# Kernel optimization log

Hardware: AMD Instinct MI355X
Metric: run time of the kernel (lower is better)

Reference implementation:

```python
import jax, jax.numpy as jnp
import numpy as np

B, C, H, W = 8, 64, 128, 128


def setup_inputs() -> dict:
    key = jax.random.key(0)
    k1, k2, k3 = jax.random.split(key, 3)
    x = jax.random.normal(k1, (B, C, H, W), dtype=jnp.float32)
    # offset conv weights: (2C, C, 3, 3), small init like the module (std=0.01)
    W_off = jax.random.normal(k2, (2 * C, C, 3, 3), dtype=jnp.float32) * 0.01
    # following regular conv: (C_out, C, 3, 3)
    W_conv = jax.random.normal(k3, (C, C, 3, 3), dtype=jnp.float32) * 0.05
    b_conv = jnp.zeros((C,), dtype=jnp.float32)
    return {"x": x, "W_off": W_off, "W_conv": W_conv, "b_conv": b_conv}


def _conv2d_same(x, w):
    return jax.lax.conv_general_dilated(
        x, w, window_strides=(1, 1), padding=[(1, 1), (1, 1)],
        dimension_numbers=("NCHW", "OIHW", "NCHW"))


def _deform_offset(x, W_off):
    """Faithful ConvOffset2D: offset conv + clamped 4-corner bilinear gather."""
    b, c, h, w = x.shape
    offsets_ = _conv2d_same(x, W_off)                    # (b, 2c, h, w)
    # torch contiguous view (b,2c,h,w) -> (b*c, h*w, 2): adjacent w elements
    # become the 2 offset components; jnp.reshape matches this exactly.
    offsets = offsets_.reshape(b * c, h * w, 2)
    xf = x.reshape(b * c, h, w)

    gy, gx = jnp.meshgrid(jnp.arange(h), jnp.arange(w), indexing="ij")
    grid = jnp.stack([gy, gx], axis=-1).reshape(-1, 2).astype(x.dtype)  # (h*w, 2)
    coords = offsets + grid[None]                        # (b*c, h*w, 2)

    cy = jnp.clip(coords[..., 0], 0.0, h - 1)
    cx = jnp.clip(coords[..., 1], 0.0, w - 1)
    y0 = jnp.floor(cy)
    y1 = jnp.ceil(cy)
    x0 = jnp.floor(cx)
    x1 = jnp.ceil(cx)

    flat = xf.reshape(-1)                                # (b*c*h*w,)
    base = (jnp.arange(b * c, dtype=jnp.int32) * (h * w))[:, None]

    def gather(yy, xx):
        idx = base + yy.astype(jnp.int32) * w + xx.astype(jnp.int32)
        return flat[idx]

    v_lt = gather(y0, x0)   # (floor y, floor x)
    v_rb = gather(y1, x1)   # (ceil y,  ceil x)
    v_lb = gather(y0, x1)   # (floor y, ceil x)
    v_rt = gather(y1, x0)   # (ceil y,  floor x)

    dy = cy - y0
    dx = cx - x0
    v_t = dy * (v_rt - v_lt) + v_lt
    v_b = dy * (v_rb - v_lb) + v_lb
    out = dx * (v_b - v_t) + v_t                         # (b*c, h*w)
    return out.reshape(b, c, h, w)


def reference(x, W_off, W_conv, b_conv):
    x_def = _deform_offset(x, W_off)
    out = _conv2d_same(x_def, W_conv) + b_conv[None, :, None, None]
    return out
```

## Files before the change

### kernel.cpp

```cpp
#include <hip/hip_runtime.h>

#define DH 128
#define DW 128
#define DB 8
#define DC 64
constexpr int HW = DH * DW;

typedef __attribute__((ext_vector_type(4))) float f32x4;
typedef __attribute__((ext_vector_type(16))) float f32x16;
typedef __attribute__((ext_vector_type(8))) short bf16x8;
typedef __attribute__((ext_vector_type(4))) unsigned int u32x4;

__device__ __forceinline__ unsigned short f2b(float f) {
    unsigned int u = __builtin_bit_cast(unsigned int, f);
    u = (u + 0x7FFFu + ((u >> 16) & 1u)) >> 16;
    return (unsigned short)u;
}
__device__ __forceinline__ float b2f(unsigned short h) {
    unsigned int u = ((unsigned int)h) << 16;
    return __builtin_bit_cast(float, u);
}

__global__ __launch_bounds__(256) void prep_kernel(
    const float* __restrict__ x, const float* __restrict__ wo,
    const float* __restrict__ wc, unsigned short* __restrict__ xh,
    unsigned short* __restrict__ wt1, unsigned short* __restrict__ wt2)
{
    __shared__ unsigned short smx[64 * 80];
    const int blk = blockIdx.x;
    const int t = threadIdx.x;
    if (blk < 2048) {
        const int b = blk >> 8;
        const int p0 = (blk & 255) * 64;
        const int ci = t >> 2, q = t & 3;
        const float* xr = x + ((size_t)b * 64 + ci) * HW + p0;
#pragma unroll
        for (int j = 0; j < 4; ++j) {
            int pix = (j * 4 + q) * 4;
            float4 v = *(const float4*)(xr + pix);
            smx[(pix + 0) * 80 + ci] = f2b(v.x);
            smx[(pix + 1) * 80 + ci] = f2b(v.y);
            smx[(pix + 2) * 80 + ci] = f2b(v.z);
            smx[(pix + 3) * 80 + ci] = f2b(v.w);
        }
        __syncthreads();
        unsigned short* outp = xh + ((size_t)b * HW + p0) * 64;
        for (int i = t; i < 512; i += 256) {
            int pix = i >> 3, cq = i & 7;
            u32x4 v = *(const u32x4*)(smx + pix * 80 + cq * 8);
            *(u32x4*)(outp + pix * 64 + cq * 8) = v;
        }
    } else {
        int id = (blk - 2048) * 256 + t;
        const int N1 = 9 * 128 * 64, N2 = 9 * 64 * 64;
        if (id < N1) {
            int c8 = id & 7, r = id >> 3;
            int cr = r & 31; r >>= 5;
            int h = r & 1; r >>= 1;
            int kk = r & 3; r >>= 2;
            int cb = r & 3; int tp = r >> 2;
            int co = cb * 32 + cr, ci = kk * 16 + h * 8 + c8;
            wt1[id] = f2b(wo[(co * 64 + ci) * 9 + tp]);
        } else if (id < N1 + N2) {
            int k = id - N1;
            int c8 = k & 7, r = k >> 3;
            int cr = r & 31; r >>= 5;
            int h = r & 1; r >>= 1;
            int kk = r & 3; r >>= 2;
            int cb = r & 1; int tp = r >> 1;
            int co = cb * 32 + cr, ci = kk * 16 + h * 8 + c8;
            wt2[k] = f2b(wc[(co * 64 + ci) * 9 + tp]);
        }
    }
}

__global__ __launch_bounds__(512, 4) void conv1_kernel(
    const unsigned short* __restrict__ xh,
    const unsigned short* __restrict__ wt,
    unsigned short* __restrict__ outp)
{
    __shared__ char sm[41472];
    const int tid = threadIdx.x;
    const int b = blockIdx.y;
    const int ty0 = (blockIdx.x >> 3) << 4;
    const int tx0 = (blockIdx.x & 7) << 4;
    const unsigned short* xb = xh + (size_t)b * HW * 64;

    for (int i = tid; i < 2592; i += 512) {
        int hp = i >> 3, cq = i & 7;
        int hy = hp / 18, hx = hp - hy * 18;
        int gy = ty0 + hy - 1, gx = tx0 + hx - 1;
        u32x4 v = {0u, 0u, 0u, 0u};
        if ((unsigned)gy < 128u && (unsigned)gx < 128u)
            v = *(const u32x4*)(xb + (size_t)((gy << 7) + gx) * 64 + cq * 8);
        *(u32x4*)(sm + ((hp * 128 + cq * 16) ^ ((hp & 7) << 4))) = v;
    }
    __syncthreads();

    const int lane = tid & 63;
    const int wv = tid >> 6;
    const int wq = wv & 3;
    const int wc = wv >> 2;
    const int n = lane & 31;
    const int half = lane >> 5;
    const int px = n & 15;
    const int pyb = wq * 4 + (n >> 4);

    int hp0[2];
#pragma unroll
    for (int pi = 0; pi < 2; ++pi)
        hp0[pi] = (pyb + pi * 2) * 18 + px;

    f32x16 acc[2][2];
#pragma unroll
    for (int pi = 0; pi < 2; ++pi)
#pragma unroll
        for (int cj = 0; cj < 2; ++cj)
#pragma unroll
            for (int e = 0; e < 16; ++e) acc[pi][cj][e] = 0.f;

#pragma unroll
    for (int t9 = 0; t9 < 9; ++t9) {
        const int toff = (t9 / 3) * 18 + (t9 % 3);
        bf16x8 w[2][4];
#pragma unroll
        for (int cj = 0; cj < 2; ++cj)
#pragma unroll
            for (int kk = 0; kk < 4; ++kk)
                w[cj][kk] = *(const bf16x8*)(wt +
                    (size_t)((((t9 * 4 + wc * 2 + cj) * 4 + kk) * 2 + half) * 32 + n) * 8);
#pragma unroll
        for (int kk = 0; kk < 4; ++kk) {
            bf16x8 a[2];
#pragma unroll
            for (int pi = 0; pi < 2; ++pi) {
                int hp = hp0[pi] + toff;
                a[pi] = *(const bf16x8*)(sm + ((hp * 128 + kk * 32 + half * 16) ^ ((hp & 7) << 4)));
            }
#pragma unroll
            for (int pi = 0; pi < 2; ++pi)
#pragma unroll
                for (int cj = 0; cj < 2; ++cj)
                    acc[pi][cj] = __builtin_amdgcn_mfma_f32_32x32x16_bf16(
                        a[pi], w[cj][kk], acc[pi][cj], 0, 0, 0);
        }
    }

    unsigned short* obp = outp + (size_t)b * HW * 128;
#pragma unroll
    for (int pi = 0; pi < 2; ++pi)
#pragma unroll
        for (int cj = 0; cj < 2; ++cj) {
            int cob = (wc * 2 + cj) * 32 + n;
#pragma unroll
            for (int r = 0; r < 16; ++r) {
                int m = (r & 3) + 8 * (r >> 2) + 4 * half;
                int py = wq * 4 + pi * 2 + (m >> 4);
                int gp = (ty0 + py) * 128 + tx0 + (m & 15);
                obp[(size_t)gp * 128 + cob] = f2b(acc[pi][cj][r]);
            }
        }
}

__global__ __launch_bounds__(512, 4) void conv2_deform_kernel(
    const unsigned short* __restrict__ xh,
    const unsigned short* __restrict__ offs,
    const unsigned short* __restrict__ wt,
    const float* __restrict__ bias,
    float* __restrict__ out)
{
    __shared__ char sm[41472];
    const int tid = threadIdx.x;
    const int b = blockIdx.y;
    const int ty0 = (blockIdx.x >> 3) << 4;
    const int tx0 = (blockIdx.x & 7) << 4;
    const unsigned short* xb = xh + (size_t)b * HW * 64;
    const unsigned short* ob = offs + (size_t)b * HW * 128;

    auto deform_one = [&](int i) {
        int hp = i >> 6, ci = i & 63;
        int hy = hp / 18, hx = hp - hy * 18;
        int gy = ty0 + hy - 1, gx = tx0 + hx - 1;
        unsigned short val = 0;
        if ((unsigned)gy < 128u && (unsigned)gx < 128u) {
            int q = (gy << 7) + gx;
            int ch = 2 * ci + (q >> 13);
            int pp = (2 * q) & (HW - 1);
            float oy = b2f(ob[(size_t)pp * 128 + ch]);
            float ox = b2f(ob[(size_t)(pp + 1) * 128 + ch]);
            float cy = fminf(fmaxf(oy + (float)gy, 0.f), 127.f);
            float cx = fminf(fmaxf(ox + (float)gx, 0.f), 127.f);
            float y0f = floorf(cy), x0f = floorf(cx);
            int y0 = (int)y0f, x0i = (int)x0f;
            int y1 = (int)ceilf(cy), x1 = (int)ceilf(cx);
            const unsigned short* pl = xb + ci;
            float v_lt = b2f(pl[(size_t)(y0 * 128 + x0i) * 64]);
            float v_rb = b2f(pl[(size_t)(y1 * 128 + x1) * 64]);
            float v_lb = b2f(pl[(size_t)(y0 * 128 + x1) * 64]);
            float v_rt = b2f(pl[(size_t)(y1 * 128 + x0i) * 64]);
            float dy = cy - y0f, dxf = cx - x0f;
            float v_t = fmaf(dy, v_rt - v_lt, v_lt);
            float v_b = fmaf(dy, v_rb - v_lb, v_lb);
            val = f2b(fmaf(dxf, v_b - v_t, v_t));
        }
        *(unsigned short*)(sm + ((hp * 128 + ci * 2) ^ ((hp & 7) << 4))) = val;
    };
#pragma unroll 4
    for (int k = 0; k < 40; ++k) deform_one(tid + k * 512);
    if (tid < 256) deform_one(tid + 40 * 512);
    __syncthreads();

    const int lane = tid & 63;
    const int wv = tid >> 6;
    const int wm = wv & 1;
    const int wn = wv >> 1;
    const int n = lane & 31;
    const int half = lane >> 5;
    const int px = n & 15;
    const int pyb = wn * 4 + (n >> 4);

    int hp0[2];
#pragma unroll
    for (int ni = 0; ni < 2; ++ni)
        hp0[ni] = (pyb + ni * 2) * 18 + px;

    f32x16 acc[2];
#pragma unroll
    for (int ni = 0; ni < 2; ++ni)
#pragma unroll
        for (int e = 0; e < 16; ++e) acc[ni][e] = 0.f;

#pragma unroll
    for (int t9 = 0; t9 < 9; ++t9) {
        const int toff = (t9 / 3) * 18 + (t9 % 3);
        bf16x8 a[4];
#pragma unroll
        for (int kk = 0; kk < 4; ++kk)
            a[kk] = *(const bf16x8*)(wt +
                (size_t)((((t9 * 2 + wm) * 4 + kk) * 2 + half) * 32 + n) * 8);
#pragma unroll
        for (int kk = 0; kk < 4; ++kk) {
            bf16x8 bv[2];
#pragma unroll
            for (int ni = 0; ni < 2; ++ni) {
                int hp = hp0[ni] + toff;
                bv[ni] = *(const bf16x8*)(sm + ((hp * 128 + kk * 32 + half * 16) ^ ((hp & 7) << 4)));
            }
#pragma unroll
            for (int ni = 0; ni < 2; ++ni)
                acc[ni] = __builtin_amdgcn_mfma_f32_32x32x16_bf16(
                    a[kk], bv[ni], acc[ni], 0, 0, 0);
        }
    }

#pragma unroll
    for (int ni = 0; ni < 2; ++ni) {
        int gp = (ty0 + pyb + ni * 2) * 128 + tx0 + px;
        float* o = out + (size_t)b * 64 * HW + gp;
        int cob = wm * 32 + half * 4;
#pragma unroll
        for (int g = 0; g < 4; ++g)
#pragma unroll
            for (int r = 0; r < 4; ++r) {
                int co = cob + g * 8 + r;
                o[(size_t)co * HW] = acc[ni][g * 4 + r] + bias[co];
            }
    }
}

extern "C" void kernel_launch(void* const* d_in, const int* in_sizes, int n_in,
                              void* d_out, int out_size, void* d_ws, size_t ws_size,
                              hipStream_t stream) {
    const float* x      = (const float*)d_in[0];
    const float* W_off  = (const float*)d_in[1];
    const float* W_conv = (const float*)d_in[2];
    const float* b_conv = (const float*)d_in[3];

    unsigned short* xh   = (unsigned short*)d_ws;
    unsigned short* offs = xh + (size_t)DB * HW * 64;
    unsigned short* wt1  = offs + (size_t)DB * HW * 128;
    unsigned short* wt2  = wt1 + 9 * 128 * 64;
    float* out = (float*)d_out;

    prep_kernel<<<2048 + 432, 256, 0, stream>>>(x, W_off, W_conv, xh, wt1, wt2);

    conv1_kernel<<<dim3(64, DB), 512, 0, stream>>>(xh, wt1, offs);

    conv2_deform_kernel<<<dim3(64, DB), 512, 0, stream>>>(
        xh, offs, wt2, b_conv, out);
}
```

Baseline: 183.1 us.

## Store offset conv output in deform-ready packed (oy,ox) layout via shared-memory transpose

The offset convolution epilogue now stages results through shared memory and writes them so that the (oy, ox) pair each deform sample needs sits in one 32-bit word, indexed by pixel and channel. The deform gather then does a single coalesced 32-bit load instead of two scattered 16-bit loads. This trades extra syncthreads and an LDS round trip in conv1 for cheaper, coalesced offset reads in conv2, and also replaces conv1's scattered 2-byte global stores with coalesced 4-byte stores.

```diff
diff --git a/kernel.cpp b/kernel.cpp
--- a/kernel.cpp
+++ b/kernel.cpp
@@ -77,7 +77,7 @@
 __global__ __launch_bounds__(512, 4) void conv1_kernel(
     const unsigned short* __restrict__ xh,
     const unsigned short* __restrict__ wt,
-    unsigned short* __restrict__ outp)
+    unsigned int* __restrict__ offsu)
 {
     __shared__ char sm[41472];
     const int tid = threadIdx.x;
@@ -146,25 +146,42 @@
         }
     }
 
-    unsigned short* obp = outp + (size_t)b * HW * 128;
-#pragma unroll
-    for (int pi = 0; pi < 2; ++pi)
-#pragma unroll
-        for (int cj = 0; cj < 2; ++cj) {
-            int cob = (wc * 2 + cj) * 32 + n;
-#pragma unroll
-            for (int r = 0; r < 16; ++r) {
-                int m = (r & 3) + 8 * (r >> 2) + 4 * half;
-                int py = wq * 4 + pi * 2 + (m >> 4);
-                int gp = (ty0 + py) * 128 + tx0 + (m & 15);
-                obp[(size_t)gp * 128 + cob] = f2b(acc[pi][cj][r]);
-            }
-        }
+    __syncthreads();
+    unsigned int* ou = offsu + (size_t)b * HW * 64;
+#pragma unroll
+    for (int ph = 0; ph < 2; ++ph) {
+        if ((wq >> 1) == ph) {
+#pragma unroll
+            for (int pi = 0; pi < 2; ++pi)
+#pragma unroll
+                for (int cj = 0; cj < 2; ++cj) {
+                    int ch = (wc * 2 + cj) * 32 + n;
+#pragma unroll
+                    for (int r = 0; r < 16; ++r) {
+                        int m = (r & 3) + 8 * (r >> 2) + 4 * half;
+                        int py8 = (wq & 1) * 4 + pi * 2 + (m >> 4);
+                        int pxx = m & 15;
+                        int idx = (py8 * 8 + (pxx >> 1)) * 256 + ch * 2 + (pxx & 1);
+                        *(unsigned short*)(sm + idx * 2) = f2b(acc[pi][cj][r]);
+                    }
+                }
+        }
+        __syncthreads();
+#pragma unroll
+        for (int j = 0; j < 16; ++j) {
+            int f = j * 512 + tid;
+            int py = f >> 10, hi = (f >> 9) & 1, pp = (f >> 6) & 7, ci = f & 63;
+            unsigned v = *(unsigned*)(sm + (py * 8 + pp) * 512 + (2 * ci + hi) * 4);
+            int q = hi * 8192 + (ty0 + ph * 8 + py) * 64 + (tx0 >> 1) + pp;
+            ou[(size_t)q * 64 + ci] = v;
+        }
+        if (ph == 0) __syncthreads();
+    }
 }
 
 __global__ __launch_bounds__(512, 4) void conv2_deform_kernel(
     const unsigned short* __restrict__ xh,
-    const unsigned short* __restrict__ offs,
+    const unsigned int* __restrict__ offsu,
     const unsigned short* __restrict__ wt,
     const float* __restrict__ bias,
     float* __restrict__ out)
@@ -175,7 +192,7 @@
     const int ty0 = (blockIdx.x >> 3) << 4;
     const int tx0 = (blockIdx.x & 7) << 4;
     const unsigned short* xb = xh + (size_t)b * HW * 64;
-    const unsigned short* ob = offs + (size_t)b * HW * 128;
+    const unsigned int* obu = offsu + (size_t)b * HW * 64;
 
     auto deform_one = [&](int i) {
         int hp = i >> 6, ci = i & 63;
@@ -184,10 +201,9 @@
         unsigned short val = 0;
         if ((unsigned)gy < 128u && (unsigned)gx < 128u) {
             int q = (gy << 7) + gx;
-            int ch = 2 * ci + (q >> 13);
-            int pp = (2 * q) & (HW - 1);
-            float oy = b2f(ob[(size_t)pp * 128 + ch]);
-            float ox = b2f(ob[(size_t)(pp + 1) * 128 + ch]);
+            unsigned o2 = obu[(size_t)q * 64 + ci];
+            float oy = b2f((unsigned short)(o2 & 0xffffu));
+            float ox = b2f((unsigned short)(o2 >> 16));
             float cy = fminf(fmaxf(oy + (float)gy, 0.f), 127.f);
             float cx = fminf(fmaxf(ox + (float)gx, 0.f), 127.f);
             float y0f = floorf(cy), x0f = floorf(cx);
@@ -277,15 +293,15 @@
     const float* b_conv = (const float*)d_in[3];
 
     unsigned short* xh   = (unsigned short*)d_ws;
-    unsigned short* offs = xh + (size_t)DB * HW * 64;
-    unsigned short* wt1  = offs + (size_t)DB * HW * 128;
+    unsigned int*   offsu = (unsigned int*)(xh + (size_t)DB * HW * 64);
+    unsigned short* wt1  = (unsigned short*)(offsu + (size_t)DB * HW * 64);
     unsigned short* wt2  = wt1 + 9 * 128 * 64;
     float* out = (float*)d_out;
 
     prep_kernel<<<2048 + 432, 256, 0, stream>>>(x, W_off, W_conv, xh, wt1, wt2);
 
-    conv1_kernel<<<dim3(64, DB), 512, 0, stream>>>(xh, wt1, offs);
+    conv1_kernel<<<dim3(64, DB), 512, 0, stream>>>(xh, wt1, offsu);
 
     conv2_deform_kernel<<<dim3(64, DB), 512, 0, stream>>>(
-        xh, offs, wt2, b_conv, out);
-}
+        xh, offsu, wt2, b_conv, out);
+}
```

Result: faster. 164.1 us (-10.4%).
